# Performance work log

Hardware: AMD Instinct MI355X
Metric: run time of the kernel (lower is better)

## Reference

```python
import jax, jax.numpy as jnp
import numpy as np

D_MODEL = 256; D_FFN = 1024; N_LEVELS = 4; N_HEADS = 8; N_POINTS = 4; N_VT = 8
D_HEAD = D_MODEL // N_HEADS
SHAPES = [(64, 64), (32, 32), (16, 16), (8, 8)]
L_SP = sum(h * w for h, w in SHAPES)  # 5440
BATCH = 4
EPS = 1e-5


def _ln(x, g, b):
    m = jnp.mean(x, -1, keepdims=True)
    xc = x - m
    v = jnp.mean(xc * xc, -1, keepdims=True)
    return g * xc * jax.lax.rsqrt(v + EPS) + b


def _bilinear(v_flat, x, y, H, W):
    # v_flat: (N, H*W, M, Dh); x, y: (N, Q, M) pixel coords (align_corners=False, zero padding)
    x0 = jnp.floor(x); y0 = jnp.floor(y)
    wx = x - x0; wy = y - y0
    out = 0.0
    for cx, cy, w in ((x0, y0, (1 - wx) * (1 - wy)), (x0 + 1, y0, wx * (1 - wy)),
                      (x0, y0 + 1, (1 - wx) * wy), (x0 + 1, y0 + 1, wx * wy)):
        valid = (cx >= 0) & (cx < W) & (cy >= 0) & (cy < H)
        xi = jnp.clip(cx, 0, W - 1).astype(jnp.int32)
        yi = jnp.clip(cy, 0, H - 1).astype(jnp.int32)
        idx = (yi * W + xi)[..., None]  # (N, Q, M, 1)
        g = jnp.take_along_axis(v_flat, idx, axis=1)  # (N, Q, M, Dh)
        out = out + (w * valid)[..., None] * g
    return out


def _msdeform_attn(query, ref, value_in, shapes_np, pad_mask, Wv, bv, Wo, bo, Wa, ba, Wp, bp):
    N, Lq, D = query.shape
    M, Lv, P, Dh = N_HEADS, N_LEVELS, N_POINTS, D_HEAD
    value = value_in @ Wv.T + bv
    value = jnp.where(pad_mask[..., None], 0.0, value)
    value = value.reshape(N, Lq, M, Dh)
    off = (query @ Wo.T + bo).reshape(N, Lq, M, Lv, P, 2)
    attn = jax.nn.softmax((query @ Wa.T + ba).reshape(N, Lq, M, Lv * P), axis=-1)
    attn = attn.reshape(N, Lq, M, Lv, P)
    # offset normalizer is (W, H) per level
    normalizer = jnp.asarray([[w, h] for h, w in shapes_np], jnp.float32)
    loc = ref[:, :, None, :, None, :] + off / normalizer[None, None, None, :, None, :]
    out = 0.0
    start = 0
    for l, (H, W) in enumerate(shapes_np):
        v_l = value[:, start:start + H * W]  # (N, H*W, M, Dh)
        x = (loc[:, :, :, l, :, 0] * W - 0.5).transpose(0, 1, 3, 2).reshape(N, Lq * P, M)
        y = (loc[:, :, :, l, :, 1] * H - 0.5).transpose(0, 1, 3, 2).reshape(N, Lq * P, M)
        samp = _bilinear(v_l, x, y, H, W).reshape(N, Lq, P, M, Dh)
        out = out + jnp.einsum('nqpmd,nqmp->nqmd', samp, attn[:, :, :, l, :])
        start += H * W
    return out.reshape(N, Lq, D) @ Wp.T + bp


def setup_inputs() -> dict:
    key = jax.random.key(0)
    ks = jax.random.split(key, 16)
    N, D = BATCH, D_MODEL
    Lq = L_SP + N_VT
    s = D ** -0.5
    rn = lambda k, sh, sc=1.0: jax.random.normal(k, sh, dtype=jnp.float32) * sc
    starts = np.cumsum([0] + [h * w for h, w in SHAPES[:-1]])
    return {
        'src': rn(ks[0], (N, L_SP, D)),
        'pos': rn(ks[1], (N, L_SP, D), 0.1),
        'reference_points': jax.random.uniform(ks[2], (N, Lq, N_LEVELS, 2), dtype=jnp.float32),
        'spatial_shapes': jnp.asarray(SHAPES, jnp.int32),
        'level_start_index': jnp.asarray(starts, jnp.int32),
        'padding_mask': jnp.zeros((N, Lq), bool),
        'all_vt': rn(ks[3], (N, 75 * N_VT, D)),
        'sel_vt': rn(ks[4], (N, N_VT, D)),
        'W_value': rn(ks[5], (D, D), s), 'b_value': jnp.zeros((D,), jnp.float32),
        'W_off': rn(ks[6], (N_HEADS * N_LEVELS * N_POINTS * 2, D), s),
        'b_off': rn(ks[7], (N_HEADS * N_LEVELS * N_POINTS * 2,), 0.1),
        'W_attn': rn(ks[8], (N_HEADS * N_LEVELS * N_POINTS, D), s),
        'b_attn': jnp.zeros((N_HEADS * N_LEVELS * N_POINTS,), jnp.float32),
        'W_out': rn(ks[9], (D, D), s), 'b_out': jnp.zeros((D,), jnp.float32),
        'g1': jnp.ones((D,), jnp.float32), 'beta1': jnp.zeros((D,), jnp.float32),
        'W1': rn(ks[10], (D_FFN, D), s), 'bf1': jnp.zeros((D_FFN,), jnp.float32),
        'W2': rn(ks[11], (D, D_FFN), D_FFN ** -0.5), 'bf2': jnp.zeros((D,), jnp.float32),
        'g2': jnp.ones((D,), jnp.float32), 'beta2': jnp.zeros((D,), jnp.float32),
    }


def reference(src, pos, reference_points, spatial_shapes, level_start_index, padding_mask,
              all_vt, sel_vt, W_value, b_value, W_off, b_off, W_attn, b_attn, W_out, b_out,
              g1, beta1, W1, bf1, W2, bf2, g2, beta2):
    shapes_np = [tuple(int(v) for v in row) for row in np.asarray(spatial_shapes)]
    q = jnp.concatenate([src + pos, sel_vt], axis=1)      # (N, Lq, D)
    v_in = jnp.concatenate([src, sel_vt], axis=1)
    src2 = _msdeform_attn(q, reference_points, v_in, shapes_np, padding_mask,
                          W_value, b_value, W_off, b_off, W_attn, b_attn, W_out, b_out)
    x = _ln(v_in + src2, g1, beta1)
    h = jax.nn.relu(x @ W1.T + bf1) @ W2.T + bf2
    x = _ln(x + h, g2, beta2)
    return (x[:, :L_SP, :], all_vt, x[:, L_SP:, :])
```

## Files before the change

kernel.cpp:

```cpp
#include <hip/hip_runtime.h>
#include <math.h>

#define NB   4
#define LQ   5448
#define LSP  5440
#define NR   21792
#define DM   256

typedef unsigned short u16;
typedef __attribute__((ext_vector_type(8))) short short8;
typedef __attribute__((ext_vector_type(4))) float f32x4;
typedef __attribute__((ext_vector_type(4))) unsigned int uint4v;

__device__ __forceinline__ u16 f2bf(float f) {
  unsigned int u = __float_as_uint(f);
  u = (u + 0x7fff + ((u >> 16) & 1)) >> 16;
  return (u16)u;
}
__device__ __forceinline__ float bf2f(u16 u) {
  return __uint_as_float(((unsigned int)u) << 16);
}
__device__ __forceinline__ uint4v pack8(float4 a, float4 b) {
  uint4v r;
  r.x = (unsigned)f2bf(a.x) | ((unsigned)f2bf(a.y) << 16);
  r.y = (unsigned)f2bf(a.z) | ((unsigned)f2bf(a.w) << 16);
  r.z = (unsigned)f2bf(b.x) | ((unsigned)f2bf(b.y) << 16);
  r.w = (unsigned)f2bf(b.z) | ((unsigned)f2bf(b.w) << 16);
  return r;
}

#define OFF_R0 0ull
#define OFF_R1 44630016ull
#define OFF_R2 55787520ull
#define OFF_R3 66945024ull
#define OFF_WB 78102528ull
#define OFF_BI 79609856ull

#define WOF_V  0
#define WOF_OA 65536
#define WOF_P  163840
#define WOF_1  229376
#define WOF_2  491520
#define NWELEM 753664

#define OUT0 5570560ull
#define OUT1 614400ull

__global__ __launch_bounds__(256) void convw_k(
    const float* __restrict__ Wv, const float* __restrict__ Wo,
    const float* __restrict__ Wa, const float* __restrict__ Wp,
    const float* __restrict__ W1, const float* __restrict__ W2,
    const float* __restrict__ bo, const float* __restrict__ ba,
    u16* __restrict__ out, float* __restrict__ boa)
{
  const int gid = blockIdx.x * 256 + threadIdx.x;
  if (gid < 384) boa[gid] = (gid < 256) ? bo[gid] : ba[gid - 256];
  if (gid >= NWELEM) return;
  float v;
  if (gid < WOF_OA) {
    v = Wv[gid];
  } else if (gid < WOF_P) {
    const int o = gid - WOF_OA;
    v = (o < 65536) ? Wo[o] : Wa[o - 65536];
  } else if (gid < WOF_1) {
    v = Wp[gid - WOF_P];
  } else if (gid < WOF_2) {
    v = W1[gid - WOF_1];
  } else {
    v = W2[gid - WOF_2];
  }
  out[gid] = f2bf(v);
}

template <int AMODE, int EPI, int BN, int NITER>
__global__ __launch_bounds__(BN) void gemmP(
    const u16* __restrict__ A, int lda,
    const float* __restrict__ src, const float* __restrict__ pos,
    const float* __restrict__ sel,
    const u16* __restrict__ B, int ldb,
    const float* __restrict__ bias, int K,
    u16* __restrict__ outb, int ldob,
    const u16* __restrict__ xbf,
    const float* __restrict__ gvec, const float* __restrict__ bvec,
    float* __restrict__ outf, int ldof)
{
  constexpr int NW = BN / 64;
  __shared__ u16 As[32 * 256];
  __shared__ u16 Bs[NW * 4096];
  const int tid = threadIdx.x;
  const int w = tid >> 6, lane = tid & 63;
  const int l15 = lane & 15, quad = lane >> 4;
  const int m0 = blockIdx.y * 32;
  const int n0 = blockIdx.x * (BN * NITER);
  const int swz = (quad ^ ((l15 >> 1) & 3)) * 8;

  const int rA = (tid & 127) >> 2;
  const int pA = tid & 3;
  const int jb = ((tid >> 7) & 1) * 4;
  const int cA = (pA ^ ((rA >> 1) & 3)) * 8;
  const int ldsA = rA * 32 + pA * 8;
  int gmA = m0 + rA; if (gmA >= NR) gmA = NR - 1;
  const float* aV = nullptr; const float* aP = nullptr;
  if (AMODE) {
    const int n = gmA / LQ, i = gmA - n * LQ;
    if (i < LSP) {
      aV = src + ((size_t)(n * LSP + i)) * DM;
      if (AMODE == 1) aP = pos + ((size_t)(n * LSP + i)) * DM;
    } else {
      aV = sel + ((size_t)(n * 8 + (i - LSP))) * DM;
    }
  }

  int rB[4], cB[4], lB[4];
#pragma unroll
  for (int i = 0; i < 4; ++i) {
    const int g = lane + i * 64;
    rB[i] = g >> 2;
    const int p = g & 3;
    cB[i] = (p ^ ((rB[i] >> 1) & 3)) * 8;
    lB[i] = w * 4096 + rB[i] * 32 + p * 8;
  }

  for (int it = 0; it < NITER; ++it) {
    const u16* Brow = B + (size_t)(n0 + it * BN + w * 64) * ldb;
    f32x4 acc[2][4] = {};

    for (int kc = 0; kc < K; kc += 256) {
      if (NITER == 1 || it == 0) {
        if (kc) __syncthreads();
        if (tid < 256) {
          if (AMODE == 0) {
            const u16* ap = A + (size_t)gmA * lda + kc + cA;
            uint4v t0 = *(const uint4v*)(ap + (jb + 0) * 32);
            uint4v t1 = *(const uint4v*)(ap + (jb + 1) * 32);
            uint4v t2 = *(const uint4v*)(ap + (jb + 2) * 32);
            uint4v t3 = *(const uint4v*)(ap + (jb + 3) * 32);
            *(uint4v*)&As[(jb + 0) * 1024 + ldsA] = t0;
            *(uint4v*)&As[(jb + 1) * 1024 + ldsA] = t1;
            *(uint4v*)&As[(jb + 2) * 1024 + ldsA] = t2;
            *(uint4v*)&As[(jb + 3) * 1024 + ldsA] = t3;
          } else {
#pragma unroll
            for (int i = 0; i < 4; i += 2) {
              const int j0 = jb + i, j1 = jb + i + 1;
              float4 v0a = *(const float4*)(aV + kc + j0 * 32 + cA);
              float4 v0b = *(const float4*)(aV + kc + j0 * 32 + cA + 4);
              float4 v1a = *(const float4*)(aV + kc + j1 * 32 + cA);
              float4 v1b = *(const float4*)(aV + kc + j1 * 32 + cA + 4);
              if (AMODE == 1 && aP) {
                const float4 p0a = *(const float4*)(aP + kc + j0 * 32 + cA);
                const float4 p0b = *(const float4*)(aP + kc + j0 * 32 + cA + 4);
                const float4 p1a = *(const float4*)(aP + kc + j1 * 32 + cA);
                const float4 p1b = *(const float4*)(aP + kc + j1 * 32 + cA + 4);
                v0a.x += p0a.x; v0a.y += p0a.y; v0a.z += p0a.z; v0a.w += p0a.w;
                v0b.x += p0b.x; v0b.y += p0b.y; v0b.z += p0b.z; v0b.w += p0b.w;
                v1a.x += p1a.x; v1a.y += p1a.y; v1a.z += p1a.z; v1a.w += p1a.w;
                v1b.x += p1b.x; v1b.y += p1b.y; v1b.z += p1b.z; v1b.w += p1b.w;
              }
              *(uint4v*)&As[j0 * 1024 + ldsA] = pack8(v0a, v0b);
              *(uint4v*)&As[j1 * 1024 + ldsA] = pack8(v1a, v1b);
            }
          }
        }
        __syncthreads();
      }

      uint4v rb0[4], rb1[4];
#pragma unroll
      for (int i = 0; i < 4; ++i)
        rb0[i] = *(const uint4v*)(Brow + (size_t)rB[i] * ldb + kc + cB[i]);
#pragma unroll
      for (int i = 0; i < 4; ++i)
        rb1[i] = *(const uint4v*)(Brow + (size_t)rB[i] * ldb + kc + 32 + cB[i]);
#pragma unroll
      for (int i = 0; i < 4; ++i) *(uint4v*)&Bs[lB[i]] = rb0[i];

#pragma unroll
      for (int j = 0; j < 8; ++j) {
        if (j < 6) {
          if ((j & 1) == 0) {
#pragma unroll
            for (int i = 0; i < 4; ++i)
              rb0[i] = *(const uint4v*)(Brow + (size_t)rB[i] * ldb + kc + (j + 2) * 32 + cB[i]);
          } else {
#pragma unroll
            for (int i = 0; i < 4; ++i)
              rb1[i] = *(const uint4v*)(Brow + (size_t)rB[i] * ldb + kc + (j + 2) * 32 + cB[i]);
          }
        }
        short8 af[2], bfr[4];
#pragma unroll
        for (int r = 0; r < 2; ++r)
          af[r] = *(const short8*)&As[j * 1024 + (r * 16 + l15) * 32 + swz];
#pragma unroll
        for (int c = 0; c < 4; ++c)
          bfr[c] = *(const short8*)&Bs[w * 4096 + (j & 1) * 2048 + (c * 16 + l15) * 32 + swz];
        if (j < 7) {
          const int buf = ((j + 1) & 1) * 2048;
          if ((j & 1) == 0) {
#pragma unroll
            for (int i = 0; i < 4; ++i) *(uint4v*)&Bs[lB[i] + buf] = rb1[i];
          } else {
#pragma unroll
            for (int i = 0; i < 4; ++i) *(uint4v*)&Bs[lB[i] + buf] = rb0[i];
          }
        }
#pragma unroll
        for (int r = 0; r < 2; ++r)
#pragma unroll
          for (int c = 0; c < 4; ++c)
            acc[r][c] = __builtin_amdgcn_mfma_f32_16x16x32_bf16(af[r], bfr[c], acc[r][c], 0, 0, 0);
      }
    }

    int col[4];
    float bb[4];
#pragma unroll
    for (int c = 0; c < 4; ++c) {
      col[c] = n0 + it * BN + w * 64 + c * 16 + l15;
      bb[c] = bias[col[c]];
    }

    if (EPI == 4) {
#pragma unroll
      for (int c = 0; c < 4; ++c)
#pragma unroll
        for (int r = 0; r < 2; ++r)
#pragma unroll
          for (int j = 0; j < 4; ++j) {
            const int row = m0 + r * 16 + quad * 4 + j;
            if (row < NR) outf[(size_t)row * ldof + col[c]] = acc[r][c][j] + bb[c];
          }
      continue;
    }

    if (EPI <= 1) {
#pragma unroll
      for (int c = 0; c < 4; ++c)
#pragma unroll
        for (int r = 0; r < 2; ++r)
#pragma unroll
          for (int j = 0; j < 4; ++j) {
            const int row = m0 + r * 16 + quad * 4 + j;
            if (row < NR) {
              float v = acc[r][c][j] + bb[c];
              if (EPI == 1) v = fmaxf(v, 0.f);
              outb[(size_t)row * ldob + col[c]] = f2bf(v);
            }
          }
      continue;
    }

    __syncthreads();
    float sv[2][4], sq[2][4];
#pragma unroll
    for (int r = 0; r < 2; ++r) {
#pragma unroll
      for (int j = 0; j < 4; ++j) {
        const int row = m0 + r * 16 + quad * 4 + j;
        const int rc = (row < NR) ? row : NR - 1;
        if (EPI == 2) {
          const int n = rc / LQ;
          const int i = rc - n * LQ;
          const float* resb = (i < LSP)
              ? src + ((size_t)(n * LSP + i)) * DM
              : sel + ((size_t)(n * 8 + (i - LSP))) * DM;
#pragma unroll
          for (int c = 0; c < 4; ++c) acc[r][c][j] += bb[c] + resb[col[c]];
        } else {
#pragma unroll
          for (int c = 0; c < 4; ++c)
            acc[r][c][j] += bb[c] + bf2f(xbf[(size_t)rc * DM + col[c]]);
        }
        float s = 0.f, q = 0.f;
#pragma unroll
        for (int c = 0; c < 4; ++c) {
          const float v = acc[r][c][j];
          s += v; q += v * v;
        }
        sv[r][j] = s; sq[r][j] = q;
      }
    }
#pragma unroll
    for (int off = 1; off < 16; off <<= 1) {
#pragma unroll
      for (int r = 0; r < 2; ++r)
#pragma unroll
        for (int j = 0; j < 4; ++j) {
          sv[r][j] += __shfl_xor(sv[r][j], off, 64);
          sq[r][j] += __shfl_xor(sq[r][j], off, 64);
        }
    }
    float* red = (float*)As;
    if (l15 == 0) {
#pragma unroll
      for (int r = 0; r < 2; ++r)
#pragma unroll
        for (int j = 0; j < 4; ++j) {
          const int rl = r * 16 + quad * 4 + j;
          red[(rl * 4 + w) * 2 + 0] = sv[r][j];
          red[(rl * 4 + w) * 2 + 1] = sq[r][j];
        }
    }
    __syncthreads();

    float gg[4], b2[4];
#pragma unroll
    for (int c = 0; c < 4; ++c) { gg[c] = gvec[col[c]]; b2[c] = bvec[col[c]]; }

#pragma unroll
    for (int r = 0; r < 2; ++r) {
#pragma unroll
      for (int j = 0; j < 4; ++j) {
        const int row = m0 + r * 16 + quad * 4 + j;
        if (row >= NR) continue;
        const int rl = r * 16 + quad * 4 + j;
        float ms = 0.f, mq = 0.f;
#pragma unroll
        for (int ww = 0; ww < 4; ++ww) {
          ms += red[(rl * 4 + ww) * 2 + 0];
          mq += red[(rl * 4 + ww) * 2 + 1];
        }
        const float mean = ms * (1.f / 256.f);
        const float var = mq * (1.f / 256.f) - mean * mean;
        const float rin = rsqrtf(var + 1e-5f);
        if (EPI == 2) {
#pragma unroll
          for (int c = 0; c < 4; ++c)
            outb[(size_t)row * DM + col[c]] =
                f2bf(gg[c] * (acc[r][c][j] - mean) * rin + b2[c]);
        } else {
          const int n = row / LQ;
          const int i = row - n * LQ;
          float* dst = (i < LSP)
              ? outf + (size_t)(n * LSP + i) * DM
              : outf + OUT0 + OUT1 + (size_t)(n * 8 + (i - LSP)) * DM;
#pragma unroll
          for (int c = 0; c < 4; ++c)
            dst[col[c]] = gg[c] * (acc[r][c][j] - mean) * rin + b2[c];
        }
      }
    }
  }
}

__device__ __forceinline__ void fma8(float* a, const uint4v u, float w) {
  a[0] += w * __uint_as_float(u.x << 16);
  a[1] += w * __uint_as_float(u.x & 0xffff0000u);
  a[2] += w * __uint_as_float(u.y << 16);
  a[3] += w * __uint_as_float(u.y & 0xffff0000u);
  a[4] += w * __uint_as_float(u.z << 16);
  a[5] += w * __uint_as_float(u.z & 0xffff0000u);
  a[6] += w * __uint_as_float(u.w << 16);
  a[7] += w * __uint_as_float(u.w & 0xffff0000u);
}

__global__ __launch_bounds__(256) void sample3_k(
    const u16* __restrict__ value, const float* __restrict__ oa,
    const float* __restrict__ ref, u16* __restrict__ samp)
{
  const int lb = blockIdx.x;
  const int xcd = lb & 7;
  const int idx = lb >> 3;
  const int batch = xcd >> 1;
  const int rg = idx * 2 + (xcd & 1);
  if (rg >= 681) return;
  const int lane = threadIdx.x & 63;
  const int li = threadIdx.x & 31;
  const int m = li >> 2, q4 = li & 3;
  const int row = batch * LQ + rg * 8 + (threadIdx.x >> 5);

  const float* oar = oa + (size_t)row * 384;
  const float* offm = oar + m * 32;

  const float4 lg = *(const float4*)(oar + 256 + m * 16 + q4 * 4);
  float mx = fmaxf(fmaxf(lg.x, lg.y), fmaxf(lg.z, lg.w));
  mx = fmaxf(mx, __shfl_xor(mx, 1, 64));
  mx = fmaxf(mx, __shfl_xor(mx, 2, 64));
  const float e0 = __expf(lg.x - mx), e1 = __expf(lg.y - mx),
              e2 = __expf(lg.z - mx), e3 = __expf(lg.w - mx);
  float s = e0 + e1 + e2 + e3;
  s += __shfl_xor(s, 1, 64);
  s += __shfl_xor(s, 2, 64);
  const float inv = 1.f / s;
  float wp[4] = {e0 * inv, e1 * inv, e2 * inv, e3 * inv};

  float aw[4][4];
#pragma unroll
  for (int p = 0; p < 4; ++p) {
#pragma unroll
    for (int l = 0; l < 4; ++l)
      aw[l][p] = __shfl(wp[p], (lane & ~3) | l, 64);
  }

  const float4 r01 = *(const float4*)(ref + (size_t)row * 8);
  const float4 r23 = *(const float4*)(ref + (size_t)row * 8 + 4);
  const float RX[4] = {r01.x, r01.z, r23.x, r23.z};
  const float RY[4] = {r01.y, r01.w, r23.y, r23.w};
  const int HW[4] = {64, 32, 16, 8};
  const int ST[4] = {0, 4096, 5120, 5376};

  float a[8] = {};
#pragma unroll
  for (int l = 0; l < 4; ++l) {
    const int W = HW[l];
    const float rx = RX[l], ry = RY[l];
    const u16* vb = value + ((size_t)(batch * LQ + ST[l])) * DM + m * 32 + q4 * 8;
    const float4 oA = *(const float4*)(offm + l * 8);
    const float4 oB = *(const float4*)(offm + l * 8 + 4);
    const float ox[4] = {oA.x, oA.z, oB.x, oB.z};
    const float oy[4] = {oA.y, oA.w, oB.y, oB.w};
#pragma unroll
    for (int p = 0; p < 4; ++p) {
      const float px = rx * (float)W + ox[p] - 0.5f;
      const float py = ry * (float)W + oy[p] - 0.5f;
      const float xf = floorf(px), yf = floorf(py);
      const float wx = px - xf, wy = py - yf;
      const int x0 = (int)xf, y0 = (int)yf;
      const int x1 = x0 + 1, y1 = y0 + 1;
      const float vx0 = ((x0 >= 0) & (x0 < W)) ? 1.f : 0.f;
      const float vx1 = ((x1 >= 0) & (x1 < W)) ? 1.f : 0.f;
      const float vy0 = ((y0 >= 0) & (y0 < W)) ? 1.f : 0.f;
      const float vy1 = ((y1 >= 0) & (y1 < W)) ? 1.f : 0.f;
      const int cx0 = min(max(x0, 0), W - 1), cx1 = min(max(x1, 0), W - 1);
      const int cy0 = min(max(y0, 0), W - 1), cy1 = min(max(y1, 0), W - 1);
      const float awp = aw[l][p];
      const float w00 = awp * (1.f - wx) * (1.f - wy) * vx0 * vy0;
      const float w01 = awp * wx * (1.f - wy) * vx1 * vy0;
      const float w10 = awp * (1.f - wx) * wy * vx0 * vy1;
      const float w11 = awp * wx * wy * vx1 * vy1;
      const uint4v v00 = *(const uint4v*)(vb + (size_t)(cy0 * W + cx0) * DM);
      const uint4v v01 = *(const uint4v*)(vb + (size_t)(cy0 * W + cx1) * DM);
      const uint4v v10 = *(const uint4v*)(vb + (size_t)(cy1 * W + cx0) * DM);
      const uint4v v11 = *(const uint4v*)(vb + (size_t)(cy1 * W + cx1) * DM);
      fma8(a, v00, w00);
      fma8(a, v01, w01);
      fma8(a, v10, w10);
      fma8(a, v11, w11);
    }
  }
  uint4v ov;
  ov.x = (unsigned int)f2bf(a[0]) | ((unsigned int)f2bf(a[1]) << 16);
  ov.y = (unsigned int)f2bf(a[2]) | ((unsigned int)f2bf(a[3]) << 16);
  ov.z = (unsigned int)f2bf(a[4]) | ((unsigned int)f2bf(a[5]) << 16);
  ov.w = (unsigned int)f2bf(a[6]) | ((unsigned int)f2bf(a[7]) << 16);
  *(uint4v*)(samp + (size_t)row * DM + m * 32 + q4 * 8) = ov;
}

extern "C" void kernel_launch(void* const* d_in, const int* in_sizes, int n_in,
                              void* d_out, int out_size, void* d_ws, size_t ws_size,
                              hipStream_t stream)
{
  const float* src = (const float*)d_in[0];
  const float* pos = (const float*)d_in[1];
  const float* ref = (const float*)d_in[2];
  const float* all_vt = (const float*)d_in[6];
  const float* sel = (const float*)d_in[7];
  const float* Wv = (const float*)d_in[8];
  const float* bv = (const float*)d_in[9];
  const float* Wo = (const float*)d_in[10];
  const float* bo = (const float*)d_in[11];
  const float* Wa = (const float*)d_in[12];
  const float* ba = (const float*)d_in[13];
  const float* Wp = (const float*)d_in[14];
  const float* bp = (const float*)d_in[15];
  const float* g1 = (const float*)d_in[16];
  const float* be1 = (const float*)d_in[17];
  const float* W1 = (const float*)d_in[18];
  const float* b1 = (const float*)d_in[19];
  const float* W2 = (const float*)d_in[20];
  const float* b2 = (const float*)d_in[21];
  const float* g2 = (const float*)d_in[22];
  const float* be2 = (const float*)d_in[23];

  char* ws = (char*)d_ws;
  float* oabuf = (float*)(ws + OFF_R0);
  u16* h_bf    = (u16*)(ws + OFF_R0);
  u16* samp_bf = (u16*)(ws + OFF_R1);
  u16* x_bf    = (u16*)(ws + OFF_R2);
  u16* val_bf  = (u16*)(ws + OFF_R3);
  u16* WB      = (u16*)(ws + OFF_WB);
  float* boa   = (float*)(ws + OFF_BI);

  const dim3 b256(256), b384(384);
  const int MT32 = (NR + 31) / 32;

  convw_k<<<dim3(NWELEM / 256), b256, 0, stream>>>(
      Wv, Wo, Wa, Wp, W1, W2, bo, ba, WB, boa);
  gemmP<2, 0, 256, 1><<<dim3(1, MT32), b256, 0, stream>>>(
      nullptr, 0, src, nullptr, sel, WB + WOF_V, 256, bv, 256,
      val_bf, 256, nullptr, nullptr, nullptr, nullptr, 0);
  gemmP<1, 4, 384, 1><<<dim3(1, MT32), b384, 0, stream>>>(
      nullptr, 0, src, pos, sel, WB + WOF_OA, 256, boa, 256,
      nullptr, 0, nullptr, nullptr, nullptr, oabuf, 384);
  sample3_k<<<dim3(8 * 341), b256, 0, stream>>>(val_bf, oabuf, ref, samp_bf);
  gemmP<0, 2, 256, 1><<<dim3(1, MT32), b256, 0, stream>>>(
      samp_bf, 256, src, nullptr, sel, WB + WOF_P, 256, bp, 256,
      x_bf, 256, nullptr, g1, be1, nullptr, 0);
  gemmP<0, 1, 256, 4><<<dim3(1, MT32), b256, 0, stream>>>(
      x_bf, 256, nullptr, nullptr, nullptr, WB + WOF_1, 256, b1, 256,
      h_bf, 1024, nullptr, nullptr, nullptr, nullptr, 0);
  gemmP<0, 3, 256, 1><<<dim3(1, MT32), b256, 0, stream>>>(
      h_bf, 1024, nullptr, nullptr, nullptr, WB + WOF_2, 1024, b2, 1024,
      nullptr, 0, x_bf, g2, be2, (float*)d_out, 0);
  hipMemcpyAsync((float*)d_out + OUT0, all_vt, OUT1 * sizeof(float),
                 hipMemcpyDeviceToDevice, stream);
}
```

Baseline: 287.6 us.

## Use direct global-to-LDS loads in GEMM, packed FMA in sampler, split FFN1 grid

```diff
diff --git a/kernel.cpp b/kernel.cpp
--- a/kernel.cpp
+++ b/kernel.cpp
@@ -10,7 +10,12 @@
 typedef unsigned short u16;
 typedef __attribute__((ext_vector_type(8))) short short8;
 typedef __attribute__((ext_vector_type(4))) float f32x4;
+typedef __attribute__((ext_vector_type(2))) float f32x2;
 typedef __attribute__((ext_vector_type(4))) unsigned int uint4v;
+
+#define GLL(g, l) __builtin_amdgcn_global_load_lds(                      \
+    (const __attribute__((address_space(1))) void*)(g),                  \
+    (__attribute__((address_space(3))) void*)(l), 16, 0, 0)
 
 __device__ __forceinline__ u16 f2bf(float f) {
   unsigned int u = __float_as_uint(f);
@@ -111,14 +116,13 @@
     }
   }
 
-  int rB[4], cB[4], lB[4];
+  int rB[4], cB[4];
 #pragma unroll
   for (int i = 0; i < 4; ++i) {
     const int g = lane + i * 64;
     rB[i] = g >> 2;
     const int p = g & 3;
     cB[i] = (p ^ ((rB[i] >> 1) & 3)) * 8;
-    lB[i] = w * 4096 + rB[i] * 32 + p * 8;
   }
 
   for (int it = 0; it < NITER; ++it) {
@@ -126,20 +130,24 @@
     f32x4 acc[2][4] = {};
 
     for (int kc = 0; kc < K; kc += 256) {
-      if (NITER == 1 || it == 0) {
+      const bool doA = (NITER == 1) || (it == 0);
+      if (doA) {
         if (kc) __syncthreads();
-        if (tid < 256) {
-          if (AMODE == 0) {
-            const u16* ap = A + (size_t)gmA * lda + kc + cA;
-            uint4v t0 = *(const uint4v*)(ap + (jb + 0) * 32);
-            uint4v t1 = *(const uint4v*)(ap + (jb + 1) * 32);
-            uint4v t2 = *(const uint4v*)(ap + (jb + 2) * 32);
-            uint4v t3 = *(const uint4v*)(ap + (jb + 3) * 32);
-            *(uint4v*)&As[(jb + 0) * 1024 + ldsA] = t0;
-            *(uint4v*)&As[(jb + 1) * 1024 + ldsA] = t1;
-            *(uint4v*)&As[(jb + 2) * 1024 + ldsA] = t2;
-            *(uint4v*)&As[(jb + 3) * 1024 + ldsA] = t3;
-          } else {
+        if (AMODE == 0) {
+          if (w < 4) {
+#pragma unroll
+            for (int h = 0; h < 2; ++h) {
+              const int row = h * 16 + (lane >> 2);
+              int gm = m0 + row; if (gm >= NR) gm = NR - 1;
+              const int p = lane & 3;
+              const int cc = (p ^ ((row >> 1) & 3)) * 8;
+              const u16* g0 = A + (size_t)gm * lda + kc + (2 * w) * 32 + cc;
+              GLL(g0,      &As[(2 * w) * 1024 + h * 512]);
+              GLL(g0 + 32, &As[(2 * w + 1) * 1024 + h * 512]);
+            }
+          }
+        } else {
+          if (tid < 256) {
 #pragma unroll
             for (int i = 0; i < 4; i += 2) {
               const int j0 = jb + i, j1 = jb + i + 1;
@@ -162,32 +170,30 @@
             }
           }
         }
-        __syncthreads();
       }
 
-      uint4v rb0[4], rb1[4];
 #pragma unroll
       for (int i = 0; i < 4; ++i)
-        rb0[i] = *(const uint4v*)(Brow + (size_t)rB[i] * ldb + kc + cB[i]);
+        GLL(Brow + (size_t)rB[i] * ldb + kc + cB[i],
+            &Bs[w * 4096 + i * 512]);
 #pragma unroll
       for (int i = 0; i < 4; ++i)
-        rb1[i] = *(const uint4v*)(Brow + (size_t)rB[i] * ldb + kc + 32 + cB[i]);
-#pragma unroll
-      for (int i = 0; i < 4; ++i) *(uint4v*)&Bs[lB[i]] = rb0[i];
+        GLL(Brow + (size_t)rB[i] * ldb + kc + 32 + cB[i],
+            &Bs[w * 4096 + 2048 + i * 512]);
+
+      if (doA) {
+        if (AMODE == 0) {
+          asm volatile("s_waitcnt vmcnt(8)" ::: "memory");
+        } else {
+          asm volatile("s_waitcnt lgkmcnt(0)" ::: "memory");
+        }
+        __builtin_amdgcn_s_barrier();
+      }
 
 #pragma unroll
       for (int j = 0; j < 8; ++j) {
-        if (j < 6) {
-          if ((j & 1) == 0) {
-#pragma unroll
-            for (int i = 0; i < 4; ++i)
-              rb0[i] = *(const uint4v*)(Brow + (size_t)rB[i] * ldb + kc + (j + 2) * 32 + cB[i]);
-          } else {
-#pragma unroll
-            for (int i = 0; i < 4; ++i)
-              rb1[i] = *(const uint4v*)(Brow + (size_t)rB[i] * ldb + kc + (j + 2) * 32 + cB[i]);
-          }
-        }
+        if (j < 7) asm volatile("s_waitcnt vmcnt(4)" ::: "memory");
+        else       asm volatile("s_waitcnt vmcnt(0)" ::: "memory");
         short8 af[2], bfr[4];
 #pragma unroll
         for (int r = 0; r < 2; ++r)
@@ -195,15 +201,12 @@
 #pragma unroll
         for (int c = 0; c < 4; ++c)
           bfr[c] = *(const short8*)&Bs[w * 4096 + (j & 1) * 2048 + (c * 16 + l15) * 32 + swz];
-        if (j < 7) {
-          const int buf = ((j + 1) & 1) * 2048;
-          if ((j & 1) == 0) {
-#pragma unroll
-            for (int i = 0; i < 4; ++i) *(uint4v*)&Bs[lB[i] + buf] = rb1[i];
-          } else {
-#pragma unroll
-            for (int i = 0; i < 4; ++i) *(uint4v*)&Bs[lB[i] + buf] = rb0[i];
-          }
+        asm volatile("s_waitcnt lgkmcnt(0)" ::: "memory");
+        if (j < 6) {
+#pragma unroll
+          for (int i = 0; i < 4; ++i)
+            GLL(Brow + (size_t)rB[i] * ldb + kc + (j + 2) * 32 + cB[i],
+                &Bs[w * 4096 + (j & 1) * 2048 + i * 512]);
         }
 #pragma unroll
         for (int r = 0; r < 2; ++r)
@@ -344,15 +347,17 @@
   }
 }
 
-__device__ __forceinline__ void fma8(float* a, const uint4v u, float w) {
-  a[0] += w * __uint_as_float(u.x << 16);
-  a[1] += w * __uint_as_float(u.x & 0xffff0000u);
-  a[2] += w * __uint_as_float(u.y << 16);
-  a[3] += w * __uint_as_float(u.y & 0xffff0000u);
-  a[4] += w * __uint_as_float(u.z << 16);
-  a[5] += w * __uint_as_float(u.z & 0xffff0000u);
-  a[6] += w * __uint_as_float(u.w << 16);
-  a[7] += w * __uint_as_float(u.w & 0xffff0000u);
+__device__ __forceinline__ void fma8(f32x2* a, const uint4v u, float w) {
+  const f32x2 w2 = {w, w};
+  f32x2 t;
+  t.x = __uint_as_float(u.x << 16); t.y = __uint_as_float(u.x & 0xffff0000u);
+  a[0] += w2 * t;
+  t.x = __uint_as_float(u.y << 16); t.y = __uint_as_float(u.y & 0xffff0000u);
+  a[1] += w2 * t;
+  t.x = __uint_as_float(u.z << 16); t.y = __uint_as_float(u.z & 0xffff0000u);
+  a[2] += w2 * t;
+  t.x = __uint_as_float(u.w << 16); t.y = __uint_as_float(u.w & 0xffff0000u);
+  a[3] += w2 * t;
 }
 
 __global__ __launch_bounds__(256) void sample3_k(
@@ -400,7 +405,7 @@
   const int HW[4] = {64, 32, 16, 8};
   const int ST[4] = {0, 4096, 5120, 5376};
 
-  float a[8] = {};
+  f32x2 a[4] = {};
 #pragma unroll
   for (int l = 0; l < 4; ++l) {
     const int W = HW[l];
@@ -440,10 +445,10 @@
     }
   }
   uint4v ov;
-  ov.x = (unsigned int)f2bf(a[0]) | ((unsigned int)f2bf(a[1]) << 16);
-  ov.y = (unsigned int)f2bf(a[2]) | ((unsigned int)f2bf(a[3]) << 16);
-  ov.z = (unsigned int)f2bf(a[4]) | ((unsigned int)f2bf(a[5]) << 16);
-  ov.w = (unsigned int)f2bf(a[6]) | ((unsigned int)f2bf(a[7]) << 16);
+  ov.x = (unsigned int)f2bf(a[0].x) | ((unsigned int)f2bf(a[0].y) << 16);
+  ov.y = (unsigned int)f2bf(a[1].x) | ((unsigned int)f2bf(a[1].y) << 16);
+  ov.z = (unsigned int)f2bf(a[2].x) | ((unsigned int)f2bf(a[2].y) << 16);
+  ov.w = (unsigned int)f2bf(a[3].x) | ((unsigned int)f2bf(a[3].y) << 16);
   *(uint4v*)(samp + (size_t)row * DM + m * 32 + q4 * 8) = ov;
 }
 
@@ -497,7 +502,7 @@
   gemmP<0, 2, 256, 1><<<dim3(1, MT32), b256, 0, stream>>>(
       samp_bf, 256, src, nullptr, sel, WB + WOF_P, 256, bp, 256,
       x_bf, 256, nullptr, g1, be1, nullptr, 0);
-  gemmP<0, 1, 256, 4><<<dim3(1, MT32), b256, 0, stream>>>(
+  gemmP<0, 1, 256, 1><<<dim3(4, MT32), b256, 0, stream>>>(
       x_bf, 256, nullptr, nullptr, nullptr, WB + WOF_1, 256, b1, 256,
       h_bf, 1024, nullptr, nullptr, nullptr, nullptr, 0);
   gemmP<0, 3, 256, 1><<<dim3(1, MT32), b256, 0, stream>>>(
```

New measurement: 295.5 us. 2.7% more time.

## Split sampling levels across half-waves, add MFMA priority, widen FFN1 grid

Applied to the files above, without the earlier changes.

```diff
diff --git a/kernel.cpp b/kernel.cpp
--- a/kernel.cpp
+++ b/kernel.cpp
@@ -205,11 +205,13 @@
             for (int i = 0; i < 4; ++i) *(uint4v*)&Bs[lB[i] + buf] = rb0[i];
           }
         }
+        __builtin_amdgcn_s_setprio(1);
 #pragma unroll
         for (int r = 0; r < 2; ++r)
 #pragma unroll
           for (int c = 0; c < 4; ++c)
             acc[r][c] = __builtin_amdgcn_mfma_f32_16x16x32_bf16(af[r], bfr[c], acc[r][c], 0, 0, 0);
+        __builtin_amdgcn_s_setprio(0);
       }
     }
 
@@ -355,7 +357,7 @@
   a[7] += w * __uint_as_float(u.w & 0xffff0000u);
 }
 
-__global__ __launch_bounds__(256) void sample3_k(
+__global__ __launch_bounds__(256) void sample4_k(
     const u16* __restrict__ value, const float* __restrict__ oa,
     const float* __restrict__ ref, u16* __restrict__ samp)
 {
@@ -364,11 +366,11 @@
   const int idx = lb >> 3;
   const int batch = xcd >> 1;
   const int rg = idx * 2 + (xcd & 1);
-  if (rg >= 681) return;
   const int lane = threadIdx.x & 63;
-  const int li = threadIdx.x & 31;
+  const int hi = lane >> 5;
+  const int li = lane & 31;
   const int m = li >> 2, q4 = li & 3;
-  const int row = batch * LQ + rg * 8 + (threadIdx.x >> 5);
+  const int row = batch * LQ + rg * 4 + (threadIdx.x >> 6);
 
   const float* oar = oa + (size_t)row * 384;
   const float* offm = oar + m * 32;
@@ -385,26 +387,28 @@
   const float inv = 1.f / s;
   float wp[4] = {e0 * inv, e1 * inv, e2 * inv, e3 * inv};
 
-  float aw[4][4];
+  const int L0 = hi * 2;
+  float aw[2][4];
 #pragma unroll
   for (int p = 0; p < 4; ++p) {
 #pragma unroll
-    for (int l = 0; l < 4; ++l)
-      aw[l][p] = __shfl(wp[p], (lane & ~3) | l, 64);
+    for (int t = 0; t < 2; ++t)
+      aw[t][p] = __shfl(wp[p], (lane & ~3) | (L0 + t), 64);
   }
 
   const float4 r01 = *(const float4*)(ref + (size_t)row * 8);
   const float4 r23 = *(const float4*)(ref + (size_t)row * 8 + 4);
-  const float RX[4] = {r01.x, r01.z, r23.x, r23.z};
-  const float RY[4] = {r01.y, r01.w, r23.y, r23.w};
+  const float RXa[4] = {r01.x, r01.z, r23.x, r23.z};
+  const float RYa[4] = {r01.y, r01.w, r23.y, r23.w};
   const int HW[4] = {64, 32, 16, 8};
   const int ST[4] = {0, 4096, 5120, 5376};
 
   float a[8] = {};
 #pragma unroll
-  for (int l = 0; l < 4; ++l) {
+  for (int t = 0; t < 2; ++t) {
+    const int l = L0 + t;
     const int W = HW[l];
-    const float rx = RX[l], ry = RY[l];
+    const float rx = RXa[l], ry = RYa[l];
     const u16* vb = value + ((size_t)(batch * LQ + ST[l])) * DM + m * 32 + q4 * 8;
     const float4 oA = *(const float4*)(offm + l * 8);
     const float4 oB = *(const float4*)(offm + l * 8 + 4);
@@ -424,7 +428,7 @@
       const float vy1 = ((y1 >= 0) & (y1 < W)) ? 1.f : 0.f;
       const int cx0 = min(max(x0, 0), W - 1), cx1 = min(max(x1, 0), W - 1);
       const int cy0 = min(max(y0, 0), W - 1), cy1 = min(max(y1, 0), W - 1);
-      const float awp = aw[l][p];
+      const float awp = aw[t][p];
       const float w00 = awp * (1.f - wx) * (1.f - wy) * vx0 * vy0;
       const float w01 = awp * wx * (1.f - wy) * vx1 * vy0;
       const float w10 = awp * (1.f - wx) * wy * vx0 * vy1;
@@ -439,12 +443,17 @@
       fma8(a, v11, w11);
     }
   }
-  uint4v ov;
-  ov.x = (unsigned int)f2bf(a[0]) | ((unsigned int)f2bf(a[1]) << 16);
-  ov.y = (unsigned int)f2bf(a[2]) | ((unsigned int)f2bf(a[3]) << 16);
-  ov.z = (unsigned int)f2bf(a[4]) | ((unsigned int)f2bf(a[5]) << 16);
-  ov.w = (unsigned int)f2bf(a[6]) | ((unsigned int)f2bf(a[7]) << 16);
-  *(uint4v*)(samp + (size_t)row * DM + m * 32 + q4 * 8) = ov;
+#pragma unroll
+  for (int i = 0; i < 8; ++i) a[i] += __shfl_xor(a[i], 32, 64);
+
+  if (hi == 0) {
+    uint4v ov;
+    ov.x = (unsigned int)f2bf(a[0]) | ((unsigned int)f2bf(a[1]) << 16);
+    ov.y = (unsigned int)f2bf(a[2]) | ((unsigned int)f2bf(a[3]) << 16);
+    ov.z = (unsigned int)f2bf(a[4]) | ((unsigned int)f2bf(a[5]) << 16);
+    ov.w = (unsigned int)f2bf(a[6]) | ((unsigned int)f2bf(a[7]) << 16);
+    *(uint4v*)(samp + (size_t)row * DM + m * 32 + q4 * 8) = ov;
+  }
 }
 
 extern "C" void kernel_launch(void* const* d_in, const int* in_sizes, int n_in,
@@ -493,11 +502,11 @@
   gemmP<1, 4, 384, 1><<<dim3(1, MT32), b384, 0, stream>>>(
       nullptr, 0, src, pos, sel, WB + WOF_OA, 256, boa, 256,
       nullptr, 0, nullptr, nullptr, nullptr, oabuf, 384);
-  sample3_k<<<dim3(8 * 341), b256, 0, stream>>>(val_bf, oabuf, ref, samp_bf);
+  sample4_k<<<dim3(8 * 681), b256, 0, stream>>>(val_bf, oabuf, ref, samp_bf);
   gemmP<0, 2, 256, 1><<<dim3(1, MT32), b256, 0, stream>>>(
       samp_bf, 256, src, nullptr, sel, WB + WOF_P, 256, bp, 256,
       x_bf, 256, nullptr, g1, be1, nullptr, 0);
-  gemmP<0, 1, 256, 4><<<dim3(1, MT32), b256, 0, stream>>>(
+  gemmP<0, 1, 256, 2><<<dim3(2, MT32), b256, 0, stream>>>(
       x_bf, 256, nullptr, nullptr, nullptr, WB + WOF_1, 256, b1, 256,
       h_bf, 1024, nullptr, nullptr, nullptr, nullptr, 0);
   gemmP<0, 3, 256, 1><<<dim3(1, MT32), b256, 0, stream>>>(
```

Result: slower. 296.0 us (+2.9%).
